# Performance work log

Measured on AMD Instinct MI355X. Metric: run time of the kernel, lower is better.

Reference implementation:

```python
import jax, jax.numpy as jnp
import numpy as np

D = 256  # channel dim and CBP output dim


def setup_inputs() -> dict:
    key = jax.random.key(0)
    ks = jax.random.split(key, 14)
    B, C, H, W = 32, 256, 56, 56
    attr_num = 400
    inp = {}
    inp["entity_feature"] = jax.random.normal(ks[0], (B, C, H, W), jnp.float32)
    inp["attr_one_hot"] = jax.random.uniform(ks[1], (B, attr_num), jnp.float32)
    # textual_emb: Linear(attr_num, 256)
    inp["W_emb"] = jax.random.normal(ks[2], (D, attr_num), jnp.float32) * 0.02
    inp["b_emb"] = jnp.zeros((D,), jnp.float32)
    # conv: Conv2d(256,256,1)
    inp["conv_w"] = jax.random.normal(ks[3], (D, D), jnp.float32) * 0.02
    inp["conv_b"] = jnp.zeros((D,), jnp.float32)
    # mcb_conv1_attr: Conv2d(256,32,1)
    inp["conv1_w"] = jax.random.normal(ks[4], (32, D), jnp.float32) * 0.05
    inp["conv1_b"] = jnp.zeros((32,), jnp.float32)
    # mcb_conv2_attr: Conv2d(32,1,1)
    inp["conv2_w"] = jax.random.normal(ks[5], (1, 32), jnp.float32) * 0.1
    inp["conv2_b"] = jnp.zeros((1,), jnp.float32)
    # CompactBilinearPooling count-sketch tables (fixed random at init)
    inp["h1"] = jax.random.randint(ks[6], (D,), 0, D, jnp.int32)
    inp["h2"] = jax.random.randint(ks[7], (D,), 0, D, jnp.int32)
    inp["s1"] = (jax.random.randint(ks[8], (D,), 0, 2, jnp.int32) * 2 - 1).astype(jnp.float32)
    inp["s2"] = (jax.random.randint(ks[9], (D,), 0, 2, jnp.int32) * 2 - 1).astype(jnp.float32)
    return inp


def _sketch_matrix(h, s):
    # sparse count-sketch projection as dense [C_in, D] matrix: P[i, h[i]] = s[i]
    return jnp.zeros((D, D), jnp.float32).at[jnp.arange(D), h].add(s)


def reference(entity_feature, attr_one_hot, W_emb, b_emb, conv_w, conv_b,
              conv1_w, conv1_b, conv2_w, conv2_b, h1, h2, s1, s2):
    feature = jax.nn.relu(entity_feature)                      # [B,256,H,W]
    # textual embedding + spatially-constant 1x1 conv (identical math to
    # expanding then convolving, since the expanded tensor is constant over HxW)
    t = attr_one_hot @ W_emb.T + b_emb                         # [B,256]
    a = t @ conv_w.T + conv_b                                  # [B,256]

    # Compact Bilinear Pooling (count sketch -> FFT -> elementwise mul -> iFFT)
    P1 = _sketch_matrix(h1, s1)
    P2 = _sketch_matrix(h2, s2)
    sk1 = a @ P1                                               # [B,256], spatially constant
    sk2 = jnp.einsum('bchw,cd->bdhw', feature, P2)             # [B,256,H,W]
    fft1 = jnp.fft.rfft(sk1, n=D, axis=1)[:, :, None, None]    # [B,129,1,1]
    fft2 = jnp.fft.rfft(sk2, n=D, axis=1)                      # [B,129,H,W]
    mcb = jnp.fft.irfft(fft1 * fft2, n=D, axis=1)              # [B,256,H,W]

    # gating chain: conv1x1 -> relu -> conv1x1 -> sigmoid
    x = jax.nn.relu(jnp.einsum('bchw,oc->bohw', mcb, conv1_w) + conv1_b[None, :, None, None])
    attr_map = jax.nn.sigmoid(jnp.einsum('bchw,oc->bohw', x, conv2_w) + conv2_b[None, :, None, None])  # [B,1,H,W]
    attr_feature = attr_map * entity_feature                   # [B,256,H,W]
    return attr_map, attr_feature
```

## Files before the change

### kernel.cpp

```cpp
#include <hip/hip_runtime.h>

#define Dq   256
#define ATTR 400
#define HW   3136
#define NB   32

typedef __attribute__((ext_vector_type(8))) short bf16x8;
typedef __attribute__((ext_vector_type(4))) float f32x4;

__device__ __forceinline__ unsigned short f2bf(float f) {
  unsigned int x = __float_as_uint(f);
  return (unsigned short)((x + 0x7FFFu + ((x >> 16) & 1u)) >> 16);
}

__global__ __launch_bounds__(256) void k_sk1(
    const float* __restrict__ oh, const float* __restrict__ W_emb,
    const float* __restrict__ b_emb, const float* __restrict__ conv_w,
    const float* __restrict__ conv_b, const int* __restrict__ h1,
    const float* __restrict__ s1, float* __restrict__ sk1_out) {
  __shared__ float ohs[ATTR];
  __shared__ float ts[Dq];
  __shared__ float sk[Dq];
  const int b = blockIdx.x, tid = threadIdx.x;
  for (int j = tid; j < ATTR; j += 256) ohs[j] = oh[b * ATTR + j];
  sk[tid] = 0.f;
  __syncthreads();
  float acc = b_emb[tid];
  const float* wr = W_emb + tid * ATTR;
  for (int j = 0; j < ATTR; ++j) acc = fmaf(ohs[j], wr[j], acc);
  ts[tid] = acc;
  __syncthreads();
  float a = conv_b[tid];
  const float* cr = conv_w + tid * Dq;
  for (int k = 0; k < Dq; ++k) a = fmaf(ts[k], cr[k], a);
  atomicAdd(&sk[h1[tid]], a * s1[tid]);
  __syncthreads();
  sk1_out[b * Dq + tid] = sk[tid];
}

__global__ __launch_bounds__(256) void k_G(
    const float* __restrict__ sk1, const float* __restrict__ conv1_w,
    const int* __restrict__ h2, const float* __restrict__ s2,
    unsigned short* __restrict__ Abuf) {
  __shared__ float sks[Dq];
  __shared__ float w1[Dq];
  __shared__ float Tl[Dq];
  const int b = blockIdx.x >> 5, o = blockIdx.x & 31, c = threadIdx.x;
  sks[c] = sk1[b * Dq + c];
  w1[c]  = conv1_w[o * Dq + c];
  __syncthreads();
  float t = 0.f;
  for (int d = 0; d < Dq; ++d) t = fmaf(w1[d], sks[(d - c) & 255], t);
  Tl[c] = t;
  __syncthreads();
  const float g = s2[c] * Tl[h2[c]];
  const int frag = (o >> 4) * 8 + (c >> 5);
  const int lane = (o & 15) | (((c >> 3) & 3) << 4);
  Abuf[(((size_t)b * 16 + frag) * 64 + lane) * 8 + (c & 7)] = f2bf(g);
}

__global__ __launch_bounds__(64) void k_fused(
    const float* __restrict__ ent,
    const unsigned short* __restrict__ Abuf,
    const float* __restrict__ c1b, const float* __restrict__ c2w,
    const float* __restrict__ c2b,
    float* __restrict__ out)
{
  const int b = blockIdx.y, l = threadIdx.x;
  const int n = l & 15, kg = l >> 4;
  const int px_base = blockIdx.x * 64;

  const float* ep = ent + (size_t)b * Dq * HW + px_base + 4 * n;
  const unsigned short* Ab = Abuf + ((size_t)b * 16 * 64 + l) * 8;

  f32x4 acc[4][2];
#pragma unroll
  for (int q = 0; q < 4; ++q) { acc[q][0] = f32x4{0,0,0,0}; acc[q][1] = f32x4{0,0,0,0}; }

#pragma unroll
  for (int ks = 0; ks < 8; ++ks) {
    f32x4 f[8];
#pragma unroll
    for (int j = 0; j < 8; ++j)
      f[j] = *reinterpret_cast<const f32x4*>(ep + (size_t)(ks * 32 + kg * 8 + j) * HW);

    bf16x8 a0 = *reinterpret_cast<const bf16x8*>(Ab + (size_t)(0 * 8 + ks) * 64 * 8);
    bf16x8 a1 = *reinterpret_cast<const bf16x8*>(Ab + (size_t)(1 * 8 + ks) * 64 * 8);

#pragma unroll
    for (int q = 0; q < 4; ++q) {
      bf16x8 bv;
#pragma unroll
      for (int j = 0; j < 8; ++j) bv[j] = (short)f2bf(fmaxf(f[j][q], 0.f));
      acc[q][0] = __builtin_amdgcn_mfma_f32_16x16x32_bf16(a0, bv, acc[q][0], 0, 0, 0);
      acc[q][1] = __builtin_amdgcn_mfma_f32_16x16x32_bf16(a1, bv, acc[q][1], 0, 0, 0);
    }
  }

  const float4 b1a = reinterpret_cast<const float4*>(c1b)[kg];
  const float4 b1b = reinterpret_cast<const float4*>(c1b)[kg + 4];
  const float4 w2a = reinterpret_cast<const float4*>(c2w)[kg];
  const float4 w2b = reinterpret_cast<const float4*>(c2w)[kg + 4];
  const float c2b0 = c2b[0];

  f32x4 s4;
#pragma unroll
  for (int q = 0; q < 4; ++q) {
    float z = 0.f;
    z = fmaf(w2a.x, fmaxf(acc[q][0][0] + b1a.x, 0.f), z);
    z = fmaf(w2a.y, fmaxf(acc[q][0][1] + b1a.y, 0.f), z);
    z = fmaf(w2a.z, fmaxf(acc[q][0][2] + b1a.z, 0.f), z);
    z = fmaf(w2a.w, fmaxf(acc[q][0][3] + b1a.w, 0.f), z);
    z = fmaf(w2b.x, fmaxf(acc[q][1][0] + b1b.x, 0.f), z);
    z = fmaf(w2b.y, fmaxf(acc[q][1][1] + b1b.y, 0.f), z);
    z = fmaf(w2b.z, fmaxf(acc[q][1][2] + b1b.z, 0.f), z);
    z = fmaf(w2b.w, fmaxf(acc[q][1][3] + b1b.w, 0.f), z);
    z += __shfl_xor(z, 16);
    z += __shfl_xor(z, 32);
    s4[q] = 1.f / (1.f + __expf(-(z + c2b0)));
  }

  if (l < 16)
    *reinterpret_cast<f32x4*>(out + (size_t)b * HW + px_base + 4 * l) = s4;

  const size_t fbase = (size_t)NB * HW + (size_t)b * Dq * HW + px_base + 4 * n;
  float* fp = out + fbase;
#pragma unroll 8
  for (int cc = 0; cc < 64; ++cc) {
    const size_t off = (size_t)(kg * 64 + cc) * HW;
    f32x4 e = *reinterpret_cast<const f32x4*>(ep + off);
    *reinterpret_cast<f32x4*>(fp + off) = e * s4;
  }
}

extern "C" void kernel_launch(void* const* d_in, const int* in_sizes, int n_in,
                              void* d_out, int out_size, void* d_ws, size_t ws_size,
                              hipStream_t stream) {
  const float* ent    = (const float*)d_in[0];
  const float* oh     = (const float*)d_in[1];
  const float* W_emb  = (const float*)d_in[2];
  const float* b_emb  = (const float*)d_in[3];
  const float* conv_w = (const float*)d_in[4];
  const float* conv_b = (const float*)d_in[5];
  const float* c1w    = (const float*)d_in[6];
  const float* c1b    = (const float*)d_in[7];
  const float* c2w    = (const float*)d_in[8];
  const float* c2b    = (const float*)d_in[9];
  const int*   h1     = (const int*)d_in[10];
  const int*   h2     = (const int*)d_in[11];
  const float* s1     = (const float*)d_in[12];
  const float* s2     = (const float*)d_in[13];

  float* ws  = (float*)d_ws;
  float* sk1 = ws;
  unsigned short* Abuf = (unsigned short*)(ws + NB * Dq);

  hipLaunchKernelGGL(k_sk1, dim3(NB), dim3(256), 0, stream,
                     oh, W_emb, b_emb, conv_w, conv_b, h1, s1, sk1);
  hipLaunchKernelGGL(k_G, dim3(NB * 32), dim3(256), 0, stream,
                     sk1, c1w, h2, s2, Abuf);
  hipLaunchKernelGGL(k_fused, dim3(49, NB), dim3(64), 0, stream,
                     ent, Abuf, c1b, c2w, c2b, (float*)d_out);
}
```

Before: 80.62 us.

## Split fused kernel K-reduction across four waves with LDS atomic reduction

The fused gating kernel goes from one wave per 64-pixel tile to four waves. Each wave handles a quarter of the channel reduction for the MFMA GEMM, and partial accumulators are combined through shared-memory atomics. The output multiply loop is also split across the four waves. This targets latency and low occupancy from long serial per-wave loops, at the cost of LDS atomics and extra barriers.

Measured after the change: 127.6 us. 1.58x slower.

```diff
diff --git a/kernel.cpp b/kernel.cpp
--- a/kernel.cpp
+++ b/kernel.cpp
@@ -59,16 +59,20 @@
   Abuf[(((size_t)b * 16 + frag) * 64 + lane) * 8 + (c & 7)] = f2bf(g);
 }
 
-__global__ __launch_bounds__(64) void k_fused(
+__global__ __launch_bounds__(256) void k_fused(
     const float* __restrict__ ent,
     const unsigned short* __restrict__ Abuf,
     const float* __restrict__ c1b, const float* __restrict__ c2w,
     const float* __restrict__ c2b,
     float* __restrict__ out)
 {
-  const int b = blockIdx.y, l = threadIdx.x;
+  __shared__ float red[32][64];
+  const int b = blockIdx.y, tid = threadIdx.x;
+  const int w = tid >> 6, l = tid & 63;
   const int n = l & 15, kg = l >> 4;
   const int px_base = blockIdx.x * 64;
+
+  for (int i = tid; i < 2048; i += 256) (&red[0][0])[i] = 0.f;
 
   const float* ep = ent + (size_t)b * Dq * HW + px_base + 4 * n;
   const unsigned short* Ab = Abuf + ((size_t)b * 16 * 64 + l) * 8;
@@ -77,15 +81,18 @@
 #pragma unroll
   for (int q = 0; q < 4; ++q) { acc[q][0] = f32x4{0,0,0,0}; acc[q][1] = f32x4{0,0,0,0}; }
 
+  __syncthreads();
+
 #pragma unroll
-  for (int ks = 0; ks < 8; ++ks) {
+  for (int ks = 0; ks < 2; ++ks) {
+    const int ksg = w * 2 + ks;
     f32x4 f[8];
 #pragma unroll
     for (int j = 0; j < 8; ++j)
-      f[j] = *reinterpret_cast<const f32x4*>(ep + (size_t)(ks * 32 + kg * 8 + j) * HW);
+      f[j] = *reinterpret_cast<const f32x4*>(ep + (size_t)(ksg * 32 + kg * 8 + j) * HW);
 
-    bf16x8 a0 = *reinterpret_cast<const bf16x8*>(Ab + (size_t)(0 * 8 + ks) * 64 * 8);
-    bf16x8 a1 = *reinterpret_cast<const bf16x8*>(Ab + (size_t)(1 * 8 + ks) * 64 * 8);
+    bf16x8 a0 = *reinterpret_cast<const bf16x8*>(Ab + (size_t)(0 * 8 + ksg) * 64 * 8);
+    bf16x8 a1 = *reinterpret_cast<const bf16x8*>(Ab + (size_t)(1 * 8 + ksg) * 64 * 8);
 
 #pragma unroll
     for (int q = 0; q < 4; ++q) {
@@ -97,6 +104,15 @@
     }
   }
 
+#pragma unroll
+  for (int q = 0; q < 4; ++q)
+#pragma unroll
+    for (int t = 0; t < 2; ++t)
+#pragma unroll
+      for (int r = 0; r < 4; ++r)
+        atomicAdd(&red[q * 8 + t * 4 + r][l], acc[q][t][r]);
+  __syncthreads();
+
   const float4 b1a = reinterpret_cast<const float4*>(c1b)[kg];
   const float4 b1b = reinterpret_cast<const float4*>(c1b)[kg + 4];
   const float4 w2a = reinterpret_cast<const float4*>(c2w)[kg];
@@ -107,27 +123,27 @@
 #pragma unroll
   for (int q = 0; q < 4; ++q) {
     float z = 0.f;
-    z = fmaf(w2a.x, fmaxf(acc[q][0][0] + b1a.x, 0.f), z);
-    z = fmaf(w2a.y, fmaxf(acc[q][0][1] + b1a.y, 0.f), z);
-    z = fmaf(w2a.z, fmaxf(acc[q][0][2] + b1a.z, 0.f), z);
-    z = fmaf(w2a.w, fmaxf(acc[q][0][3] + b1a.w, 0.f), z);
-    z = fmaf(w2b.x, fmaxf(acc[q][1][0] + b1b.x, 0.f), z);
-    z = fmaf(w2b.y, fmaxf(acc[q][1][1] + b1b.y, 0.f), z);
-    z = fmaf(w2b.z, fmaxf(acc[q][1][2] + b1b.z, 0.f), z);
-    z = fmaf(w2b.w, fmaxf(acc[q][1][3] + b1b.w, 0.f), z);
+    z = fmaf(w2a.x, fmaxf(red[q * 8 + 0][l] + b1a.x, 0.f), z);
+    z = fmaf(w2a.y, fmaxf(red[q * 8 + 1][l] + b1a.y, 0.f), z);
+    z = fmaf(w2a.z, fmaxf(red[q * 8 + 2][l] + b1a.z, 0.f), z);
+    z = fmaf(w2a.w, fmaxf(red[q * 8 + 3][l] + b1a.w, 0.f), z);
+    z = fmaf(w2b.x, fmaxf(red[q * 8 + 4][l] + b1b.x, 0.f), z);
+    z = fmaf(w2b.y, fmaxf(red[q * 8 + 5][l] + b1b.y, 0.f), z);
+    z = fmaf(w2b.z, fmaxf(red[q * 8 + 6][l] + b1b.z, 0.f), z);
+    z = fmaf(w2b.w, fmaxf(red[q * 8 + 7][l] + b1b.w, 0.f), z);
     z += __shfl_xor(z, 16);
     z += __shfl_xor(z, 32);
     s4[q] = 1.f / (1.f + __expf(-(z + c2b0)));
   }
 
-  if (l < 16)
+  if (tid < 16)
     *reinterpret_cast<f32x4*>(out + (size_t)b * HW + px_base + 4 * l) = s4;
 
-  const size_t fbase = (size_t)NB * HW + (size_t)b * Dq * HW + px_base + 4 * n;
-  float* fp = out + fbase;
-#pragma unroll 8
-  for (int cc = 0; cc < 64; ++cc) {
-    const size_t off = (size_t)(kg * 64 + cc) * HW;
+  const size_t fb = (size_t)NB * HW + (size_t)b * Dq * HW + px_base + 4 * n;
+  float* fp = out + fb;
+#pragma unroll 4
+  for (int cc = 0; cc < 16; ++cc) {
+    const size_t off = (size_t)(w * 64 + kg * 16 + cc) * HW;
     f32x4 e = *reinterpret_cast<const f32x4*>(ep + off);
     *reinterpret_cast<f32x4*>(fp + off) = e * s4;
   }
@@ -159,6 +175,6 @@
                      oh, W_emb, b_emb, conv_w, conv_b, h1, s1, sk1);
   hipLaunchKernelGGL(k_G, dim3(NB * 32), dim3(256), 0, stream,
                      sk1, c1w, h2, s2, Abuf);
-  hipLaunchKernelGGL(k_fused, dim3(49, NB), dim3(64), 0, stream,
+  hipLaunchKernelGGL(k_fused, dim3(HW / 64, NB), dim3(256), 0, stream,
                      ent, Abuf, c1b, c2w, c2b, (float*)d_out);
 }
```
